# Performance work log

Hardware: AMD Instinct MI355X
Metric: run time of the kernel (lower is better)

The kernel has to match this reference:

```python
import jax, jax.numpy as jnp
import numpy as np

D_MODEL, D_STATE, D_CONV, D_INNER, DT_RANK = 256, 128, 4, 512, 16

def _pos_encoding(L, d):
    pos = jnp.arange(L, dtype=jnp.float32)[:, None]
    div = jnp.exp(jnp.arange(0, d, 2, dtype=jnp.float32) * (-np.log(10000.0) / d))
    pe = jnp.zeros((L, d), dtype=jnp.float32)
    pe = pe.at[:, 0::2].set(jnp.sin(pos * div))
    pe = pe.at[:, 1::2].set(jnp.cos(pos * div))
    return pe

def setup_inputs() -> dict:
    key = jax.random.key(0)
    ks = jax.random.split(key, 16)
    B = 16
    s = 0.02
    inp = {
        'text': jax.random.normal(ks[0], (B, 768), jnp.float32),
        'img': jax.random.normal(ks[1], (B, 1568, 196), jnp.float32),
        'first_hidden': jax.random.normal(ks[2], (B, 3584), jnp.float32),
        'last_hidden': jax.random.normal(ks[3], (B, 3584), jnp.float32),
        'pt_w': jax.random.normal(ks[4], (D_MODEL, 768), jnp.float32) * s,
        'pt_b': jnp.zeros((D_MODEL,), jnp.float32),
        'pi_w': jax.random.normal(ks[5], (D_MODEL, 1568), jnp.float32) * s,
        'pi_b': jnp.zeros((D_MODEL,), jnp.float32),
        'pf_w': jax.random.normal(ks[6], (D_MODEL, 3584), jnp.float32) * s,
        'pf_b': jnp.zeros((D_MODEL,), jnp.float32),
        'pl_w': jax.random.normal(ks[7], (D_MODEL, 3584), jnp.float32) * s,
        'pl_b': jnp.zeros((D_MODEL,), jnp.float32),
        'in_proj_w': jax.random.normal(ks[8], (2 * D_INNER, D_MODEL), jnp.float32) * s,
        'conv_w': jax.random.normal(ks[9], (D_INNER, D_CONV), jnp.float32) * 0.1,
        'conv_b': jnp.zeros((D_INNER,), jnp.float32),
        'x_proj_w': jax.random.normal(ks[10], (DT_RANK + 2 * D_STATE, D_INNER), jnp.float32) * s,
        'dt_proj_w': jax.random.normal(ks[11], (D_INNER, DT_RANK), jnp.float32) * (DT_RANK ** -0.5),
        'dt_proj_b': jnp.log(jnp.expm1(jnp.full((D_INNER,), 0.01, jnp.float32))),
        'A_log': jnp.broadcast_to(jnp.log(jnp.arange(1, D_STATE + 1, dtype=jnp.float32)), (D_INNER, D_STATE)).copy(),
        'Dp': jnp.ones((D_INNER,), jnp.float32),
        'out_proj_w': jax.random.normal(ks[12], (D_MODEL, D_INNER), jnp.float32) * s,
    }
    return inp

def _mamba(seq, in_proj_w, conv_w, conv_b, x_proj_w, dt_proj_w, dt_proj_b, A_log, Dp, out_proj_w):
    B, L, _ = seq.shape
    xz = seq @ in_proj_w.T                       # [B, L, 2*dI]
    x, z = jnp.split(xz, 2, axis=-1)             # each [B, L, dI]
    # causal depthwise conv1d (kernel d_conv, left-pad)
    xp = jnp.pad(x, ((0, 0), (D_CONV - 1, 0), (0, 0)))
    xc = sum(xp[:, k:k + L, :] * conv_w[:, k] for k in range(D_CONV)) + conv_b
    x = jax.nn.silu(xc)
    dbc = x @ x_proj_w.T                         # [B, L, dt_rank + 2*dS]
    dt = dbc[..., :DT_RANK]
    Bm = dbc[..., DT_RANK:DT_RANK + D_STATE]
    Cm = dbc[..., DT_RANK + D_STATE:]
    delta = jax.nn.softplus(dt @ dt_proj_w.T + dt_proj_b)  # [B, L, dI]
    A = -jnp.exp(A_log)                          # [dI, dS]

    def step(h, inp):
        d_t, x_t, b_t, c_t = inp                 # [B,dI],[B,dI],[B,dS],[B,dS]
        dA = jnp.exp(d_t[..., None] * A)         # [B, dI, dS]
        h = dA * h + (d_t * x_t)[..., None] * b_t[:, None, :]
        y = jnp.einsum('bds,bs->bd', h, c_t)
        return h, y

    h0 = jnp.zeros((B, D_INNER, D_STATE), seq.dtype)
    xs = (jnp.swapaxes(delta, 0, 1), jnp.swapaxes(x, 0, 1),
          jnp.swapaxes(Bm, 0, 1), jnp.swapaxes(Cm, 0, 1))
    _, ys = jax.lax.scan(step, h0, xs)           # ys: [L, B, dI]
    y = jnp.swapaxes(ys, 0, 1) + x * Dp
    y = y * jax.nn.silu(z)
    return y @ out_proj_w.T

def reference(text, img, first_hidden, last_hidden, pt_w, pt_b, pi_w, pi_b,
              pf_w, pf_b, pl_w, pl_b, in_proj_w, conv_w, conv_b, x_proj_w,
              dt_proj_w, dt_proj_b, A_log, Dp, out_proj_w):
    t = (text @ pt_w.T + pt_b)[:, None, :]                       # [B,1,256]
    im = jnp.swapaxes(img, 1, 2) @ pi_w.T + pi_b                 # [B,196,256]
    f = (first_hidden @ pf_w.T + pf_b)[:, None, :]
    l = (last_hidden @ pl_w.T + pl_b)[:, None, :]
    seq = jnp.concatenate([t, im, f, l], axis=1)                 # [B,199,256]
    seq = seq + _pos_encoding(seq.shape[1], D_MODEL)[None]
    residual = seq
    out = _mamba(seq, in_proj_w, conv_w, conv_b, x_proj_w,
                 dt_proj_w, dt_proj_b, A_log, Dp, out_proj_w)
    return out + residual
```

## Files before the change

kernel.cpp:

```cpp
#include <hip/hip_runtime.h>
#include <hip/hip_bf16.h>
#include <math.h>

#define D_MODEL 256
#define D_STATE 128
#define D_CONV  4
#define D_INNER 512
#define DT_RANK 16
#define BATCH   16
#define LIMG    196
#define LSEQ    199
#define KTXT    768
#define KIMG    1568
#define KHID    3584
#define N_TOK   (BATCH*LSEQ)
#define N_IMG   (BATCH*LIMG)

typedef const float* fp32p;
typedef __attribute__((ext_vector_type(8))) short bf16x8;
typedef __attribute__((ext_vector_type(4))) float f32x4;
typedef __attribute__((ext_vector_type(2))) float f32x2;

__device__ __forceinline__ unsigned short f2bf(float f) {
    unsigned int u = __float_as_uint(f);
    u += 0x7FFFu + ((u >> 16) & 1u);
    return (unsigned short)(u >> 16);
}

__device__ __forceinline__ float bf2f(unsigned short u) {
    return __uint_as_float(((unsigned int)u) << 16);
}

#define KCH 256
__global__ __launch_bounds__(256) void cvt_embed_kernel(
    fp32p inp_w, fp32p pi_w, fp32p xp_w, fp32p out_w, fp32p dt_w,
    unsigned short* __restrict__ inp_o, unsigned short* __restrict__ pi_o,
    unsigned short* __restrict__ xp_o, unsigned short* __restrict__ out_o,
    unsigned short* __restrict__ dt_o,
    fp32p text, fp32p firsth, fp32p lasth,
    fp32p pt_w, fp32p pf_w, fp32p pl_w,
    float* __restrict__ ppart)
{
    __shared__ __align__(16) float As[32][20];
    __shared__ __align__(16) float Ws[32][68];
    if (blockIdx.x < 928) {
        int i = (blockIdx.x * 256 + threadIdx.x) * 4;
        if (i >= 950272) return;
        if (i >= 933888) {
            int q = (i - 933888) >> 2;
            int n = q >> 3, kq = q & 7;
            int k = 4 * kq;
            ushort4 o;
            if (k < DT_RANK) {
                float4 v = *(const float4*)(dt_w + (size_t)n * DT_RANK + k);
                o.x = f2bf(v.x); o.y = f2bf(v.y); o.z = f2bf(v.z); o.w = f2bf(v.w);
            } else { o.x = o.y = o.z = o.w = 0; }
            *(ushort4*)(dt_o + (size_t)n * 32 + k) = o;
            return;
        }
        const float* src; unsigned short* dst; int off;
        if (i < 262144)      { src = inp_w; dst = inp_o; off = i; }
        else if (i < 663552) { src = pi_w;  dst = pi_o;  off = i - 262144; }
        else if (i < 802816) { src = xp_w;  dst = xp_o;  off = i - 663552; }
        else                 { src = out_w; dst = out_o; off = i - 802816; }
        float4 v = *(const float4*)(src + off);
        ushort4 o;
        o.x = f2bf(v.x); o.y = f2bf(v.y); o.z = f2bf(v.z); o.w = f2bf(v.w);
        *(ushort4*)(dst + off) = o;
        return;
    }
    const int q = blockIdx.x - 928;
    const int chunk = q % 31;
    const int n0 = (q / 31) * 64;
    const float *src, *w; int k0, K;
    if (chunk < 3)       { src = text;   w = pt_w; k0 = chunk*KCH;      K = KTXT; }
    else if (chunk < 17) { src = firsth; w = pf_w; k0 = (chunk-3)*KCH;  K = KHID; }
    else                 { src = lasth;  w = pl_w; k0 = (chunk-17)*KCH; K = KHID; }

    const int tid = threadIdx.x;
    const int tm = (tid & 7) * 2;
    const int tn = (tid >> 3) * 2;
    float acc[2][2] = {{0.f,0.f},{0.f,0.f}};

    for (int ks = 0; ks < KCH; ks += 32) {
        __syncthreads();
        if (tid < 128) {
            int m = tid >> 3, kq = tid & 7;
            float4 v = *(const float4*)(src + (size_t)m*K + k0 + ks + 4*kq);
            As[4*kq+0][m]=v.x; As[4*kq+1][m]=v.y; As[4*kq+2][m]=v.z; As[4*kq+3][m]=v.w;
        }
        for (int f = tid; f < 512; f += 256) {
            int n = f >> 3, kq = f & 7;
            float4 v = *(const float4*)(w + (size_t)(n0+n)*K + k0 + ks + 4*kq);
            Ws[4*kq+0][n]=v.x; Ws[4*kq+1][n]=v.y; Ws[4*kq+2][n]=v.z; Ws[4*kq+3][n]=v.w;
        }
        __syncthreads();
        #pragma unroll
        for (int kk = 0; kk < 32; ++kk) {
            float2 a = *(const float2*)&As[kk][tm];
            float2 b = *(const float2*)&Ws[kk][tn];
            acc[0][0] = fmaf(a.x, b.x, acc[0][0]);
            acc[0][1] = fmaf(a.x, b.y, acc[0][1]);
            acc[1][0] = fmaf(a.y, b.x, acc[1][0]);
            acc[1][1] = fmaf(a.y, b.y, acc[1][1]);
        }
    }
    float* pp = ppart + (size_t)chunk*16*256;
    pp[(size_t)(tm+0)*256 + n0+tn+0] = acc[0][0];
    pp[(size_t)(tm+0)*256 + n0+tn+1] = acc[0][1];
    pp[(size_t)(tm+1)*256 + n0+tn+0] = acc[1][0];
    pp[(size_t)(tm+1)*256 + n0+tn+1] = acc[1][1];
}

__global__ __launch_bounds__(256) void mfma_dt_kernel(
    const float* __restrict__ dbc,
    const unsigned short* __restrict__ Wbf,
    fp32p dt_b, float* __restrict__ delta_T, float* __restrict__ rr_T)
{
    const int w    = threadIdx.x >> 6;
    const int lane = threadIdx.x & 63;
    const int m0   = blockIdx.x * 64 + 16 * w;
    const int n0   = blockIdx.y * 32;
    const int r15  = lane & 15;
    const int quad = lane >> 4;

    f32x4 acc0 = {0.f,0.f,0.f,0.f}, acc1 = {0.f,0.f,0.f,0.f};

    bf16x8 a = {0,0,0,0,0,0,0,0};
    if (quad < 2) {
        int m = m0 + r15;
        if (m >= N_TOK) m = N_TOK - 1;
        const float* ap = dbc + (size_t)m * 272 + quad * 8;
        float4 v0 = *(const float4*)(ap);
        float4 v1 = *(const float4*)(ap + 4);
        a[0] = (short)f2bf(v0.x); a[1] = (short)f2bf(v0.y);
        a[2] = (short)f2bf(v0.z); a[3] = (short)f2bf(v0.w);
        a[4] = (short)f2bf(v1.x); a[5] = (short)f2bf(v1.y);
        a[6] = (short)f2bf(v1.z); a[7] = (short)f2bf(v1.w);
    }
    bf16x8 b0 = *(const bf16x8*)(Wbf + (size_t)(n0 + r15     ) * 32 + quad * 8);
    bf16x8 b1 = *(const bf16x8*)(Wbf + (size_t)(n0 + r15 + 16) * 32 + quad * 8);
    acc0 = __builtin_amdgcn_mfma_f32_16x16x32_bf16(a, b0, acc0, 0, 0, 0);
    acc1 = __builtin_amdgcn_mfma_f32_16x16x32_bf16(a, b1, acc1, 0, 0, 0);

    const int mst = m0 + quad * 4;
    const int nst = n0 + r15;
    f32x4* accs[2] = {&acc0, &acc1};
    #pragma unroll
    for (int j = 0; j < 2; ++j) {
        int n = nst + 16 * j;
        float bias = dt_b[n];
        float4 o, ro;
        float* ov = &o.x; float* rv = &ro.x;
        #pragma unroll
        for (int r = 0; r < 4; ++r) {
            float v = (*accs[j])[r] + bias;
            float dlt = (v > 20.f) ? v : log1pf(__expf(v));
            ov[r] = dlt;
            rv[r] = __expf(-dlt);
        }
        if (mst + 3 < N_TOK) {
            *(float4*)(delta_T + (size_t)n * N_TOK + mst) = o;
            *(float4*)(rr_T    + (size_t)n * N_TOK + mst) = ro;
        } else {
            #pragma unroll
            for (int r = 0; r < 4; ++r)
                if (mst + r < N_TOK) {
                    delta_T[(size_t)n * N_TOK + mst + r] = ov[r];
                    rr_T   [(size_t)n * N_TOK + mst + r] = rv[r];
                }
        }
    }
}

__global__ __launch_bounds__(256) void mfma_inproj_kernel(
    const unsigned short* __restrict__ Abf,
    const unsigned short* __restrict__ Wbf,
    float* __restrict__ C, int ldc,
    fp32p conv_w, fp32p conv_b, float* __restrict__ xs_T)
{
    __shared__ __align__(16) unsigned short Ws[64][280];
    const int tid  = threadIdx.x;
    const int w    = tid >> 6;
    const int lane = tid & 63;
    const int mb   = blockIdx.x * 64;
    const int m0   = mb + 16 * w;
    const int n0   = blockIdx.y * 64;
    const int r15  = lane & 15;
    const int quad = lane >> 4;

    for (int f = tid; f < 64*32; f += 256) {
        int row = f >> 5, col = (f & 31) * 8;
        *(bf16x8*)&Ws[row][col] =
            *(const bf16x8*)(Wbf + (size_t)(n0 + row) * 256 + col);
    }
    __syncthreads();

    f32x4 acc0 = {0.f,0.f,0.f,0.f}, acc1 = {0.f,0.f,0.f,0.f};
    f32x4 acc2 = {0.f,0.f,0.f,0.f}, acc3 = {0.f,0.f,0.f,0.f};

    const unsigned short* Ap = Abf + (size_t)(m0 + r15) * 256 + quad * 8;

    #pragma unroll
    for (int k0 = 0; k0 < 256; k0 += 32) {
        bf16x8 a  = *(const bf16x8*)(Ap + k0);
        bf16x8 b0 = *(const bf16x8*)&Ws[r15     ][k0 + quad*8];
        bf16x8 b1 = *(const bf16x8*)&Ws[r15 + 16][k0 + quad*8];
        bf16x8 b2 = *(const bf16x8*)&Ws[r15 + 32][k0 + quad*8];
        bf16x8 b3 = *(const bf16x8*)&Ws[r15 + 48][k0 + quad*8];
        acc0 = __builtin_amdgcn_mfma_f32_16x16x32_bf16(a, b0, acc0, 0, 0, 0);
        acc1 = __builtin_amdgcn_mfma_f32_16x16x32_bf16(a, b1, acc1, 0, 0, 0);
        acc2 = __builtin_amdgcn_mfma_f32_16x16x32_bf16(a, b2, acc2, 0, 0, 0);
        acc3 = __builtin_amdgcn_mfma_f32_16x16x32_bf16(a, b3, acc3, 0, 0, 0);
    }

    if (n0 >= D_INNER) {
        if (m0 < N_TOK) {
            int mst = m0 + quad * 4;
            int nst = n0 + r15;
            *(float4*)(C + (size_t)(nst     ) * ldc + mst) = *(float4*)&acc0;
            *(float4*)(C + (size_t)(nst + 16) * ldc + mst) = *(float4*)&acc1;
            *(float4*)(C + (size_t)(nst + 32) * ldc + mst) = *(float4*)&acc2;
            *(float4*)(C + (size_t)(nst + 48) * ldc + mst) = *(float4*)&acc3;
        }
        return;
    }

    float halo = 0.f;
    const int htok = tid >> 6;
    const int hch  = tid & 63;
    const bool hthr = (tid < 192);
    const bool do_h = hthr && (blockIdx.x > 0);
    if (do_h) {
        int hm = mb - 3 + htok;
        const unsigned short* ar = Abf + (size_t)hm * 256;
        const unsigned short* wr = &Ws[hch][0];
        float s = 0.f;
        for (int k = 0; k < 256; k += 8) {
            bf16x8 av = *(const bf16x8*)(ar + k);
            bf16x8 wv = *(const bf16x8*)(wr + k);
            #pragma unroll
            for (int jj = 0; jj < 8; ++jj)
                s = fmaf(bf2f((unsigned short)av[jj]),
                         bf2f((unsigned short)wv[jj]), s);
        }
        halo = s;
    }
    __syncthreads();

    float* xcs = (float*)&Ws[0][0];
    #pragma unroll
    for (int r = 0; r < 4; ++r) {
        int ml = 16*w + quad*4 + r;
        xcs[(3 + ml)*68 + r15     ] = acc0[r];
        xcs[(3 + ml)*68 + r15 + 16] = acc1[r];
        xcs[(3 + ml)*68 + r15 + 32] = acc2[r];
        xcs[(3 + ml)*68 + r15 + 48] = acc3[r];
    }
    if (hthr) xcs[htok*68 + hch] = do_h ? halo : 0.f;
    __syncthreads();

    const int mst_l = 16*w + quad*4;
    #pragma unroll
    for (int j = 0; j < 4; ++j) {
        int n = n0 + r15 + 16*j;
        const int cc = r15 + 16*j;
        float w0 = conv_w[n*D_CONV + 0], w1 = conv_w[n*D_CONV + 1];
        float w2 = conv_w[n*D_CONV + 2], w3 = conv_w[n*D_CONV + 3];
        float cb = conv_b[n];
        float4 o;
        float* ov = &o.x;
        #pragma unroll
        for (int r = 0; r < 4; ++r) {
            int ml = mst_l + r;
            int m  = mb + ml;
            int tt = m % LSEQ;
            float acc = fmaf(xcs[(3+ml  )*68 + cc], w3, cb);
            if (tt >= 1) acc = fmaf(xcs[(3+ml-1)*68 + cc], w2, acc);
            if (tt >= 2) acc = fmaf(xcs[(3+ml-2)*68 + cc], w1, acc);
            if (tt >= 3) acc = fmaf(xcs[(3+ml-3)*68 + cc], w0, acc);
            float sig = 1.f / (1.f + __expf(-acc));
            ov[r] = acc * sig;
        }
        int m = mb + mst_l;
        if (m < N_TOK) {
            if (m + 3 < N_TOK) {
                *(float4*)(xs_T + (size_t)n * N_TOK + m) = o;
            } else {
                #pragma unroll
                for (int r = 0; r < 4; ++r)
                    if (m + r < N_TOK) xs_T[(size_t)n * N_TOK + m + r] = ov[r];
            }
        }
    }
}

__global__ __launch_bounds__(256) void mfma_kt_kernel(
    const float* __restrict__ Akt, int lda,
    const unsigned short* __restrict__ Wbf, int K,
    float* __restrict__ C, int ldc, int M, int N)
{
    __shared__ __align__(16) unsigned short As[2][64][40];
    const int m0 = blockIdx.x * 64;
    const int n0 = blockIdx.y * 32;
    const int tid = threadIdx.x;
    const int w = tid >> 6, lane = tid & 63;
    const int r15 = lane & 15, quad = lane >> 4;

    const int kk0 = tid >> 4,          mq0 = tid & 15;
    const int kk1 = (tid + 256) >> 4,  mq1 = (tid + 256) & 15;
    const int sm0 = m0 + 4 * mq0, sm1 = m0 + 4 * mq1;

    f32x4 acc0 = {0.f,0.f,0.f,0.f}, acc1 = {0.f,0.f,0.f,0.f};

    const unsigned short* Wp = Wbf + (size_t)(n0 + r15) * K + quad * 8;

    {
        float4 v0 = make_float4(0.f,0.f,0.f,0.f), v1 = v0;
        if (sm0 < M) v0 = *(const float4*)(Akt + (size_t)kk0 * lda + sm0);
        if (sm1 < M) v1 = *(const float4*)(Akt + (size_t)kk1 * lda + sm1);
        As[0][4*mq0+0][kk0] = f2bf(v0.x); As[0][4*mq0+1][kk0] = f2bf(v0.y);
        As[0][4*mq0+2][kk0] = f2bf(v0.z); As[0][4*mq0+3][kk0] = f2bf(v0.w);
        As[0][4*mq1+0][kk1] = f2bf(v1.x); As[0][4*mq1+1][kk1] = f2bf(v1.y);
        As[0][4*mq1+2][kk1] = f2bf(v1.z); As[0][4*mq1+3][kk1] = f2bf(v1.w);
    }
    __syncthreads();

    int p = 0;
    for (int k0 = 0; k0 < K; k0 += 32) {
        const bool hn = (k0 + 32 < K);
        float4 nv0 = make_float4(0.f,0.f,0.f,0.f), nv1 = nv0;
        if (hn) {
            if (sm0 < M) nv0 = *(const float4*)(Akt + (size_t)(k0 + 32 + kk0) * lda + sm0);
            if (sm1 < M) nv1 = *(const float4*)(Akt + (size_t)(k0 + 32 + kk1) * lda + sm1);
        }
        bf16x8 a  = *(const bf16x8*)&As[p][16*w + r15][quad * 8];
        bf16x8 b0 = *(const bf16x8*)(Wp + k0);
        bf16x8 b1 = *(const bf16x8*)(Wp + (size_t)16*K + k0);
        acc0 = __builtin_amdgcn_mfma_f32_16x16x32_bf16(a, b0, acc0, 0, 0, 0);
        acc1 = __builtin_amdgcn_mfma_f32_16x16x32_bf16(a, b1, acc1, 0, 0, 0);
        if (hn) {
            int q = p ^ 1;
            As[q][4*mq0+0][kk0] = f2bf(nv0.x); As[q][4*mq0+1][kk0] = f2bf(nv0.y);
            As[q][4*mq0+2][kk0] = f2bf(nv0.z); As[q][4*mq0+3][kk0] = f2bf(nv0.w);
            As[q][4*mq1+0][kk1] = f2bf(nv1.x); As[q][4*mq1+1][kk1] = f2bf(nv1.y);
            As[q][4*mq1+2][kk1] = f2bf(nv1.z); As[q][4*mq1+3][kk1] = f2bf(nv1.w);
        }
        __syncthreads();
        p ^= 1;
    }

    const int nb = n0 + r15;
    #pragma unroll
    for (int r = 0; r < 4; ++r) {
        int m = m0 + 16*w + quad*4 + r;
        if (m >= M) continue;
        float* cm = C + (size_t)m * ldc;
        if (nb      < N) cm[nb     ] = acc0[r];
        if (nb + 16 < N) cm[nb + 16] = acc1[r];
    }
}

__global__ __launch_bounds__(256) void mfma_out_kernel(
    const float* __restrict__ Akt,
    const unsigned short* __restrict__ Wbf,
    const float* __restrict__ seq,
    float* __restrict__ out)
{
    __shared__ __align__(16) unsigned short As[2][64][40];
    const int m0 = blockIdx.x * 64;
    const int n0 = blockIdx.y * 32;
    const int tid = threadIdx.x;
    const int w = tid >> 6, lane = tid & 63;
    const int r15 = lane & 15, quad = lane >> 4;

    const int kk0 = tid >> 4,          mq0 = tid & 15;
    const int kk1 = (tid + 256) >> 4,  mq1 = (tid + 256) & 15;
    const int sm0 = m0 + 4 * mq0, sm1 = m0 + 4 * mq1;

    f32x4 acc0 = {0.f,0.f,0.f,0.f}, acc1 = {0.f,0.f,0.f,0.f};

    const unsigned short* Wp = Wbf + (size_t)(n0 + r15) * D_INNER + quad * 8;

    {
        float4 v0 = make_float4(0.f,0.f,0.f,0.f), v1 = v0;
        if (sm0 < N_TOK) v0 = *(const float4*)(Akt + (size_t)kk0 * N_TOK + sm0);
        if (sm1 < N_TOK) v1 = *(const float4*)(Akt + (size_t)kk1 * N_TOK + sm1);
        As[0][4*mq0+0][kk0] = f2bf(v0.x); As[0][4*mq0+1][kk0] = f2bf(v0.y);
        As[0][4*mq0+2][kk0] = f2bf(v0.z); As[0][4*mq0+3][kk0] = f2bf(v0.w);
        As[0][4*mq1+0][kk1] = f2bf(v1.x); As[0][4*mq1+1][kk1] = f2bf(v1.y);
        As[0][4*mq1+2][kk1] = f2bf(v1.z); As[0][4*mq1+3][kk1] = f2bf(v1.w);
    }
    __syncthreads();

    int p = 0;
    for (int k0 = 0; k0 < D_INNER; k0 += 32) {
        const bool hn = (k0 + 32 < D_INNER);
        float4 nv0 = make_float4(0.f,0.f,0.f,0.f), nv1 = nv0;
        if (hn) {
            if (sm0 < N_TOK) nv0 = *(const float4*)(Akt + (size_t)(k0 + 32 + kk0) * N_TOK + sm0);
            if (sm1 < N_TOK) nv1 = *(const float4*)(Akt + (size_t)(k0 + 32 + kk1) * N_TOK + sm1);
        }
        bf16x8 a  = *(const bf16x8*)&As[p][16*w + r15][quad * 8];
        bf16x8 b0 = *(const bf16x8*)(Wp + k0);
        bf16x8 b1 = *(const bf16x8*)(Wp + (size_t)16*D_INNER + k0);
        acc0 = __builtin_amdgcn_mfma_f32_16x16x32_bf16(a, b0, acc0, 0, 0, 0);
        acc1 = __builtin_amdgcn_mfma_f32_16x16x32_bf16(a, b1, acc1, 0, 0, 0);
        if (hn) {
            int q = p ^ 1;
            As[q][4*mq0+0][kk0] = f2bf(nv0.x); As[q][4*mq0+1][kk0] = f2bf(nv0.y);
            As[q][4*mq0+2][kk0] = f2bf(nv0.z); As[q][4*mq0+3][kk0] = f2bf(nv0.w);
            As[q][4*mq1+0][kk1] = f2bf(nv1.x); As[q][4*mq1+1][kk1] = f2bf(nv1.y);
            As[q][4*mq1+2][kk1] = f2bf(nv1.z); As[q][4*mq1+3][kk1] = f2bf(nv1.w);
        }
        __syncthreads();
        p ^= 1;
    }

    const int nb = n0 + r15;
    #pragma unroll
    for (int r = 0; r < 4; ++r) {
        int m = m0 + 16*w + quad*4 + r;
        if (m >= N_TOK) continue;
        const float* sm = seq + (size_t)m * D_MODEL;
        float* om = out + (size_t)m * D_MODEL;
        om[nb     ] = acc0[r] + sm[nb     ];
        om[nb + 16] = acc1[r] + sm[nb + 16];
    }
}

__global__ __launch_bounds__(256) void mfma_img_kernel(
    fp32p img, const unsigned short* __restrict__ Wbf, float* __restrict__ epart)
{
    __shared__ __align__(16) unsigned short As[2][64][40];
    __shared__ __align__(16) unsigned short Ws[64][232];
    const int b  = blockIdx.x >> 2;
    const int p0 = (blockIdx.x & 3) * 64;
    const int n0 = blockIdx.y * 64;
    const int z  = blockIdx.z;
    const int tid = threadIdx.x;
    const int w = tid >> 6, lane = tid & 63;
    const int r15 = lane & 15, quad = lane >> 4;

    const int kbeg = (z == 0) ? 0 : 416 + 384 * (z - 1);
    const int kend = kbeg + ((z == 0) ? 416 : 384);
    const int hs1    = ((kend - kbeg) >> 5) >> 1;
    const int hsplit = kbeg + hs1 * 32;

    const int kk0 = tid >> 4,          pq0 = tid & 15;
    const int kk1 = (tid + 256) >> 4,  pq1 = (tid + 256) & 15;
    const int sp0 = p0 + 4 * pq0, sp1 = p0 + 4 * pq1;

    f32x4 acc0 = {0.f,0.f,0.f,0.f}, acc1 = {0.f,0.f,0.f,0.f};
    f32x4 acc2 = {0.f,0.f,0.f,0.f}, acc3 = {0.f,0.f,0.f,0.f};

    const float* imgb = img + (size_t)b * KIMG * LIMG;

    {
        float4 v0 = make_float4(0.f,0.f,0.f,0.f), v1 = v0;
        if (sp0 < LIMG) v0 = *(const float4*)(imgb + (size_t)(kbeg + kk0) * LIMG + sp0);
        if (sp1 < LIMG) v1 = *(const float4*)(imgb + (size_t)(kbeg + kk1) * LIMG + sp1);
        As[0][4*pq0+0][kk0] = f2bf(v0.x); As[0][4*pq0+1][kk0] = f2bf(v0.y);
        As[0][4*pq0+2][kk0] = f2bf(v0.z); As[0][4*pq0+3][kk0] = f2bf(v0.w);
        As[0][4*pq1+0][kk1] = f2bf(v1.x); As[0][4*pq1+1][kk1] = f2bf(v1.y);
        As[0][4*pq1+2][kk1] = f2bf(v1.z); As[0][4*pq1+3][kk1] = f2bf(v1.w);

        int cols8 = hs1 * 4;
        int tot = 64 * cols8;
        for (int f = tid; f < tot; f += 256) {
            int row = f / cols8, col = (f % cols8) * 8;
            *(bf16x8*)&Ws[row][col] =
                *(const bf16x8*)(Wbf + (size_t)(n0 + row) * KIMG + kbeg + col);
        }
    }
    __syncthreads();

    int p = 0;
    int wsbase = kbeg;
    for (int k0 = kbeg; k0 < kend; k0 += 32) {
        const bool hn = (k0 + 32 < kend);
        float4 nv0 = make_float4(0.f,0.f,0.f,0.f), nv1 = nv0;
        if (hn) {
            if (sp0 < LIMG) nv0 = *(const float4*)(imgb + (size_t)(k0 + 32 + kk0) * LIMG + sp0);
            if (sp1 < LIMG) nv1 = *(const float4*)(imgb + (size_t)(k0 + 32 + kk1) * LIMG + sp1);
        }
        const int wc = (k0 - wsbase) + quad * 8;
        bf16x8 a  = *(const bf16x8*)&As[p][16*w + r15][quad * 8];
        bf16x8 b0 = *(const bf16x8*)&Ws[r15     ][wc];
        bf16x8 b1 = *(const bf16x8*)&Ws[r15 + 16][wc];
        bf16x8 b2 = *(const bf16x8*)&Ws[r15 + 32][wc];
        bf16x8 b3 = *(const bf16x8*)&Ws[r15 + 48][wc];
        acc0 = __builtin_amdgcn_mfma_f32_16x16x32_bf16(a, b0, acc0, 0, 0, 0);
        acc1 = __builtin_amdgcn_mfma_f32_16x16x32_bf16(a, b1, acc1, 0, 0, 0);
        acc2 = __builtin_amdgcn_mfma_f32_16x16x32_bf16(a, b2, acc2, 0, 0, 0);
        acc3 = __builtin_amdgcn_mfma_f32_16x16x32_bf16(a, b3, acc3, 0, 0, 0);
        if (hn) {
            int q = p ^ 1;
            As[q][4*pq0+0][kk0] = f2bf(nv0.x); As[q][4*pq0+1][kk0] = f2bf(nv0.y);
            As[q][4*pq0+2][kk0] = f2bf(nv0.z); As[q][4*pq0+3][kk0] = f2bf(nv0.w);
            As[q][4*pq1+0][kk1] = f2bf(nv1.x); As[q][4*pq1+1][kk1] = f2bf(nv1.y);
            As[q][4*pq1+2][kk1] = f2bf(nv1.z); As[q][4*pq1+3][kk1] = f2bf(nv1.w);
        }
        __syncthreads();
        if (k0 + 32 == hsplit) {
            int cols8 = ((kend - hsplit) >> 5) * 4;
            int tot = 64 * cols8;
            for (int f = tid; f < tot; f += 256) {
                int row = f / cols8, col = (f % cols8) * 8;
                *(bf16x8*)&Ws[row][col] =
                    *(const bf16x8*)(Wbf + (size_t)(n0 + row) * KIMG + hsplit + col);
            }
            __syncthreads();
            wsbase = hsplit;
        }
        p ^= 1;
    }

    float* ep = epart + (size_t)z * N_IMG * D_MODEL;
    #pragma unroll
    for (int r = 0; r < 4; ++r) {
        int pp = p0 + 16*w + quad*4 + r;
        if (pp >= LIMG) continue;
        size_t base = ((size_t)b * LIMG + pp) * D_MODEL + n0 + r15;
        ep[base     ] = acc0[r];
        ep[base + 16] = acc1[r];
        ep[base + 32] = acc2[r];
        ep[base + 48] = acc3[r];
    }
}

__global__ __launch_bounds__(256) void finish_all_kernel(
    const float* __restrict__ epart, fp32p pi_b,
    const float* __restrict__ ppart, fp32p pt_b, fp32p pf_b, fp32p pl_b,
    float* __restrict__ seq, unsigned short* __restrict__ seq_bf)
{
    const float cpe = -9.210340371976184f / 256.0f;
    if (blockIdx.x < 784) {
        int idx = (blockIdx.x * 256 + threadIdx.x) * 4;
        int d0  = idx & (D_MODEL - 1);
        int row = idx >> 8;
        int b = row / LIMG, p = row % LIMG;
        int l = p + 1;

        float4 a0 = *(const float4*)(epart + idx);
        float4 a1 = *(const float4*)(epart + (size_t)N_IMG * D_MODEL + idx);
        float4 a2 = *(const float4*)(epart + (size_t)2 * N_IMG * D_MODEL + idx);
        float4 a3 = *(const float4*)(epart + (size_t)3 * N_IMG * D_MODEL + idx);
        float4 bb = *(const float4*)(pi_b + d0);

        float diva = __expf((float)d0 * cpe);
        float divb = __expf((float)(d0 + 2) * cpe);
        float4 o;
        o.x = (a0.x + a1.x) + (a2.x + a3.x) + bb.x + sinf((float)l * diva);
        o.y = (a0.y + a1.y) + (a2.y + a3.y) + bb.y + cosf((float)l * diva);
        o.z = (a0.z + a1.z) + (a2.z + a3.z) + bb.z + sinf((float)l * divb);
        o.w = (a0.w + a1.w) + (a2.w + a3.w) + bb.w + cosf((float)l * divb);
        size_t off = ((size_t)b * LSEQ + l) * D_MODEL + d0;
        *(float4*)(seq + off) = o;
        ushort4 ob; ob.x = f2bf(o.x); ob.y = f2bf(o.y); ob.z = f2bf(o.z); ob.w = f2bf(o.w);
        *(ushort4*)(seq_bf + off) = ob;
    } else {
        int j = (blockIdx.x - 784) * 256 + threadIdx.x;
        if (j >= 48 * 64) return;
        int d0 = (j & 63) * 4;
        int bc = j >> 6;
        int b = bc / 3, c = bc % 3;
        int c0, nch, l; const float* bias;
        if (c == 0)      { c0 = 0;  nch = 3;  l = 0;        bias = pt_b; }
        else if (c == 1) { c0 = 3;  nch = 14; l = LIMG+1;   bias = pf_b; }
        else             { c0 = 17; nch = 14; l = LIMG+2;   bias = pl_b; }
        float4 s = *(const float4*)(bias + d0);
        for (int ch = 0; ch < nch; ++ch) {
            float4 v = *(const float4*)(ppart + (size_t)(c0+ch)*16*256 + (size_t)b*256 + d0);
            s.x += v.x; s.y += v.y; s.z += v.z; s.w += v.w;
        }
        float diva = __expf((float)d0 * cpe);
        float divb = __expf((float)(d0 + 2) * cpe);
        s.x += sinf((float)l * diva);
        s.y += cosf((float)l * diva);
        s.z += sinf((float)l * divb);
        s.w += cosf((float)l * divb);
        size_t off = ((size_t)b * LSEQ + l) * D_MODEL + d0;
        *(float4*)(seq + off) = s;
        ushort4 ob; ob.x = f2bf(s.x); ob.y = f2bf(s.y); ob.z = f2bf(s.z); ob.w = f2bf(s.w);
        *(ushort4*)(seq_bf + off) = ob;
    }
}

#define TCH   16
#define NFULL 48

__global__ __launch_bounds__(256) void scan_kernel(
    const float* __restrict__ delta_T, const float* __restrict__ xs_T,
    const float* __restrict__ xz_T, const float* __restrict__ dbc_ws,
    const float* __restrict__ rr_T,
    fp32p A_log, fp32p Dp, float* __restrict__ y_T)
{
    __shared__ __align__(16) float part[4][TCH][68];
    __shared__ __align__(16) float stage[2][4][256];
    __shared__ __align__(16) float dlx[2][96];

    const int wv   = threadIdx.x >> 6;
    const int lane = threadIdx.x & 63;
    const int tid  = threadIdx.x;
    const int wid  = blockIdx.x*4 + wv;
    const int b  = wid >> 8;
    const int dp = wid & 255;
    const int sl = lane & 31;
    const int ch = lane >> 5;
    const int d  = dp*2 + ch;
    const int ch8 = (wv << 1) | ch;
    const int base_d = ((blockIdx.x*4) & 255) * 2;

    const float L2E  = 1.4426950408889634f;
    const float A0L  = -__expf(A_log[(size_t)d*D_STATE + 4*sl]) * L2E;
    const float nL2E = -L2E;

    const float* dl   = delta_T + (size_t)d*N_TOK + b*LSEQ;
    const float* xl   = xs_T    + (size_t)d*N_TOK + b*LSEQ;
    const float* dbc0 = dbc_ws  + (size_t)b*LSEQ*272 + DT_RANK;
    float* pw = &part[wv][0][0];

    const float Dr = Dp[d];
    const float* zr = xz_T + (size_t)(D_INNER + d)*N_TOK + b*LSEQ;
    float*       yr = y_T  + (size_t)d*N_TOK + b*LSEQ;

    const int  sidx = tid - 64;
    const bool do_s = (tid >= 64 && tid < 160);
    const int  s_arr = sidx >> 5, s_c8 = (sidx >> 2) & 7, s_j = sidx & 3;
    const float* s_arrp = (s_arr == 0) ? delta_T : (s_arr == 1 ? xs_T : rr_T);
    const float* s_base = s_arrp + (size_t)(base_d + s_c8)*N_TOK + b*LSEQ + s_j;

    f32x2 h01 = {0.f, 0.f}, h23 = {0.f, 0.f};

    {
        float4 bc0 = *(const float4*)(dbc0 + (size_t)wv*272 + 4*lane);
        *(float4*)&stage[0][wv][4*lane] = bc0;
        if (do_s) dlx[0][sidx] = s_base[0];
    }
    __syncthreads();

    float xt = 0.f, zt = 0.f;
    int cur = 0;
    for (int g = 0; g < NFULL; ++g) {
        const int gg = g & 3;
        if (gg == 0 && sl < TCH) {
            int t = (g >> 2)*TCH + sl;
            xt = xl[t]; zt = zr[t];
        }
        float4 bcN = *(const float4*)(dbc0 + (size_t)(4*(g+1) + wv)*272 + 4*lane);
        float dlxN = 0.f;
        if (do_s) dlxN = s_base[4*(g+1)];

        float4 dv4 = *(const float4*)&dlx[cur][     ch8*4];
        float4 xv4 = *(const float4*)&dlx[cur][32 + ch8*4];
        float4 rv4 = *(const float4*)&dlx[cur][64 + ch8*4];
        const float* sb = &stage[cur][0][0];
        #pragma unroll
        for (int j = 0; j < 4; ++j) {
            float D  = ((const float*)&dv4)[j];
            float X  = ((const float*)&xv4)[j];
            float rr = ((const float*)&rv4)[j];
            float4 Bq = *(const float4*)(sb + j*256 + 4*sl);
            float4 Cq = *(const float4*)(sb + j*256 + 128 + 4*sl);
            float du = D * X;
            float e0;
            asm("v_exp_f32 %0, %1" : "=v"(e0) : "v"(D * A0L));
            float rr2 = rr * rr;
            f32x2 e01 = {e0, e0 * rr};
            f32x2 e23 = e01 * rr2;
            f32x2 B01 = {Bq.x, Bq.y}, B23 = {Bq.z, Bq.w};
            f32x2 C01 = {Cq.x, Cq.y}, C23 = {Cq.z, Cq.w};
            h01 = e01 * h01 + du * B01;
            h23 = e23 * h23 + du * B23;
            f32x2 p2 = h01 * C01 + h23 * C23;
            pw[(gg*4 + j)*68 + lane] = p2.x + p2.y;
        }
        if (gg == 3 && sl < TCH) {
            const float* pr = pw + sl*68 + ch*32;
            float s0 = 0.f, s1 = 0.f;
            #pragma unroll
            for (int k = 0; k < 32; k += 8) {
                float4 v0 = *(const float4*)(pr + k);
                float4 v1 = *(const float4*)(pr + k + 4);
                s0 += (v0.x + v0.y) + (v0.z + v0.w);
                s1 += (v1.x + v1.y) + (v1.z + v1.w);
            }
            int t = (g >> 2)*TCH + sl;
            float y = fmaf(xt, Dr, s0 + s1);
            yr[t] = y * (zt / (1.f + __expf(-zt)));
        }
        *(float4*)&stage[cur^1][wv][4*lane] = bcN;
        if (do_s) dlx[cur^1][sidx] = dlxN;
        __syncthreads();
        cur ^= 1;
    }

    {
        const int t0 = NFULL*4, tc = LSEQ - t0;
        float xt2 = 0.f, zt2 = 0.f;
        if (sl < tc) { xt2 = xl[t0 + sl]; zt2 = zr[t0 + sl]; }
        for (int tt = 0; tt < tc; ++tt) {
            const int t = t0 + tt;
            float D = dl[t], X = xl[t];
            const float* r = dbc0 + (size_t)t*272 + 4*sl;
            float4 Bq = *(const float4*)(r);
            float4 Cq = *(const float4*)(r + D_STATE);
            float du = D * X;
            float e0, rr;
            asm("v_exp_f32 %0, %1" : "=v"(e0) : "v"(D * A0L));
            asm("v_exp_f32 %0, %1" : "=v"(rr) : "v"(D * nL2E));
            float rr2 = rr * rr;
            f32x2 e01 = {e0, e0 * rr};
            f32x2 e23 = e01 * rr2;
            f32x2 B01 = {Bq.x, Bq.y}, B23 = {Bq.z, Bq.w};
            f32x2 C01 = {Cq.x, Cq.y}, C23 = {Cq.z, Cq.w};
            h01 = e01 * h01 + du * B01;
            h23 = e23 * h23 + du * B23;
            f32x2 p2 = h01 * C01 + h23 * C23;
            pw[tt*68 + lane] = p2.x + p2.y;
        }
        if (sl < tc) {
            const float* pr = pw + sl*68 + ch*32;
            float s0 = 0.f, s1 = 0.f;
            #pragma unroll
            for (int k = 0; k < 32; k += 8) {
                float4 v0 = *(const float4*)(pr + k);
                float4 v1 = *(const float4*)(pr + k + 4);
                s0 += (v0.x + v0.y) + (v0.z + v0.w);
                s1 += (v1.x + v1.y) + (v1.z + v1.w);
            }
            float y = fmaf(xt2, Dr, s0 + s1);
            yr[t0 + sl] = y * (zt2 / (1.f + __expf(-zt2)));
        }
    }
}

extern "C" void kernel_launch(void* const* d_in, const int* in_sizes, int n_in,
                              void* d_out, int out_size, void* d_ws, size_t ws_size,
                              hipStream_t stream)
{
    fp32p text   = (fp32p)d_in[0];
    fp32p img    = (fp32p)d_in[1];
    fp32p firsth = (fp32p)d_in[2];
    fp32p lasth  = (fp32p)d_in[3];
    fp32p pt_w   = (fp32p)d_in[4];
    fp32p pt_b   = (fp32p)d_in[5];
    fp32p pi_w   = (fp32p)d_in[6];
    fp32p pi_b   = (fp32p)d_in[7];
    fp32p pf_w   = (fp32p)d_in[8];
    fp32p pf_b   = (fp32p)d_in[9];
    fp32p pl_w   = (fp32p)d_in[10];
    fp32p pl_b   = (fp32p)d_in[11];
    fp32p inp_w  = (fp32p)d_in[12];
    fp32p conv_w = (fp32p)d_in[13];
    fp32p conv_b = (fp32p)d_in[14];
    fp32p xp_w   = (fp32p)d_in[15];
    fp32p dt_w   = (fp32p)d_in[16];
    fp32p dt_b   = (fp32p)d_in[17];
    fp32p A_log  = (fp32p)d_in[18];
    fp32p Dp     = (fp32p)d_in[19];
    fp32p out_w  = (fp32p)d_in[20];

    float* ws      = (float*)d_ws;
    float* seq     = ws;
    float* xz_T    = seq     + (size_t)N_TOK*D_MODEL;
    float* xs_T    = xz_T    + (size_t)1024*N_TOK + 16;
    float* dbc_ws  = xs_T    + (size_t)D_INNER*N_TOK + 16;
    float* delta_T = dbc_ws  + (size_t)N_TOK*272;
    float* y_T     = delta_T + (size_t)D_INNER*N_TOK + 16;
    float* epart   = y_T     + (size_t)D_INNER*N_TOK + 16;
    float* ppart   = epart   + (size_t)4*N_IMG*D_MODEL;
    unsigned short* seq_bf   = (unsigned short*)(ppart + (size_t)31*16*256);
    unsigned short* inp_wbf  = seq_bf  + (size_t)3200*D_MODEL;
    unsigned short* pi_wbf   = inp_wbf + (size_t)1024*D_MODEL;
    unsigned short* xp_wbf   = pi_wbf  + (size_t)D_MODEL*KIMG;
    unsigned short* out_wbf  = xp_wbf  + (size_t)320*D_INNER;
    unsigned short* dt_wbf   = out_wbf + (size_t)D_MODEL*D_INNER;

    float* rr_T = epart;

    cvt_embed_kernel<<<1052, 256, 0, stream>>>(
        inp_w, pi_w, xp_w, out_w, dt_w, inp_wbf, pi_wbf, xp_wbf, out_wbf, dt_wbf,
        text, firsth, lasth, pt_w, pf_w, pl_w, ppart);

    mfma_img_kernel<<<dim3(BATCH*4, 4, 4), 256, 0, stream>>>(img, pi_wbf, epart);
    finish_all_kernel<<<796, 256, 0, stream>>>(
        epart, pi_b, ppart, pt_b, pf_b, pl_b, seq, seq_bf);

    mfma_inproj_kernel<<<dim3(50, 16), 256, 0, stream>>>(
        seq_bf, inp_wbf, xz_T, N_TOK, conv_w, conv_b, xs_T);

    mfma_kt_kernel<<<dim3(50, 9), 256, 0, stream>>>(
        xs_T, N_TOK, xp_wbf, D_INNER, dbc_ws, 272, N_TOK, 272);

    mfma_dt_kernel<<<dim3(50, 16), 256, 0, stream>>>(
        dbc_ws, dt_wbf, dt_b, delta_T, rr_T);

    scan_kernel<<<BATCH*D_INNER/8, 256, 0, stream>>>(
        delta_T, xs_T, xz_T, dbc_ws, rr_T, A_log, Dp, y_T);

    mfma_out_kernel<<<dim3(50, 8), 256, 0, stream>>>(
        y_T, out_wbf, seq, (float*)d_out);
}
```

Before: 255.5 us.

## Fold dt_proj into x_proj weights and compute delta inside x_proj GEMM

Precomputes a combined weight dt_proj_w @ x_proj_w[:16] (bf16, 512x512) in the conversion kernel. The x_proj GEMM grid is extended with extra column blocks that multiply xs directly by this combined weight and apply softplus and exp, so the separate dt kernel launch and its dependency on dbc are gone. The trade is that the delta GEMM's K grows from 16 to 512, which adds MFMA work. The combined weight is rounded to bf16 after the product, which changes numerics slightly.

After: 258.9 us. About the same (+1.3%).

```diff
diff --git a/kernel.cpp b/kernel.cpp
--- a/kernel.cpp
+++ b/kernel.cpp
@@ -36,7 +36,7 @@
     fp32p inp_w, fp32p pi_w, fp32p xp_w, fp32p out_w, fp32p dt_w,
     unsigned short* __restrict__ inp_o, unsigned short* __restrict__ pi_o,
     unsigned short* __restrict__ xp_o, unsigned short* __restrict__ out_o,
-    unsigned short* __restrict__ dt_o,
+    unsigned short* __restrict__ wcomb_o,
     fp32p text, fp32p firsth, fp32p lasth,
     fp32p pt_w, fp32p pf_w, fp32p pl_w,
     float* __restrict__ ppart)
@@ -45,19 +45,7 @@
     __shared__ __align__(16) float Ws[32][68];
     if (blockIdx.x < 928) {
         int i = (blockIdx.x * 256 + threadIdx.x) * 4;
-        if (i >= 950272) return;
-        if (i >= 933888) {
-            int q = (i - 933888) >> 2;
-            int n = q >> 3, kq = q & 7;
-            int k = 4 * kq;
-            ushort4 o;
-            if (k < DT_RANK) {
-                float4 v = *(const float4*)(dt_w + (size_t)n * DT_RANK + k);
-                o.x = f2bf(v.x); o.y = f2bf(v.y); o.z = f2bf(v.z); o.w = f2bf(v.w);
-            } else { o.x = o.y = o.z = o.w = 0; }
-            *(ushort4*)(dt_o + (size_t)n * 32 + k) = o;
-            return;
-        }
+        if (i >= 933888) return;
         const float* src; unsigned short* dst; int off;
         if (i < 262144)      { src = inp_w; dst = inp_o; off = i; }
         else if (i < 663552) { src = pi_w;  dst = pi_o;  off = i - 262144; }
@@ -69,6 +57,25 @@
         *(ushort4*)(dst + off) = o;
         return;
     }
+    if (blockIdx.x >= 1052) {
+        int o = ((blockIdx.x - 1052) * 256 + threadIdx.x) * 4;
+        int dd = o >> 9, k = o & 511;
+        float4 s = make_float4(0.f, 0.f, 0.f, 0.f);
+        const float* dw = dt_w + (size_t)dd * DT_RANK;
+        #pragma unroll
+        for (int r = 0; r < DT_RANK; ++r) {
+            float wv = dw[r];
+            const float* xr = xp_w + (size_t)r * D_INNER + k;
+            s.x = fmaf(wv, xr[0], s.x);
+            s.y = fmaf(wv, xr[1], s.y);
+            s.z = fmaf(wv, xr[2], s.z);
+            s.w = fmaf(wv, xr[3], s.w);
+        }
+        ushort4 ob;
+        ob.x = f2bf(s.x); ob.y = f2bf(s.y); ob.z = f2bf(s.z); ob.w = f2bf(s.w);
+        *(ushort4*)(wcomb_o + (size_t)dd * D_INNER + k) = ob;
+        return;
+    }
     const int q = blockIdx.x - 928;
     const int chunk = q % 31;
     const int n0 = (q / 31) * 64;
@@ -110,67 +117,6 @@
     pp[(size_t)(tm+0)*256 + n0+tn+1] = acc[0][1];
     pp[(size_t)(tm+1)*256 + n0+tn+0] = acc[1][0];
     pp[(size_t)(tm+1)*256 + n0+tn+1] = acc[1][1];
-}
-
-__global__ __launch_bounds__(256) void mfma_dt_kernel(
-    const float* __restrict__ dbc,
-    const unsigned short* __restrict__ Wbf,
-    fp32p dt_b, float* __restrict__ delta_T, float* __restrict__ rr_T)
-{
-    const int w    = threadIdx.x >> 6;
-    const int lane = threadIdx.x & 63;
-    const int m0   = blockIdx.x * 64 + 16 * w;
-    const int n0   = blockIdx.y * 32;
-    const int r15  = lane & 15;
-    const int quad = lane >> 4;
-
-    f32x4 acc0 = {0.f,0.f,0.f,0.f}, acc1 = {0.f,0.f,0.f,0.f};
-
-    bf16x8 a = {0,0,0,0,0,0,0,0};
-    if (quad < 2) {
-        int m = m0 + r15;
-        if (m >= N_TOK) m = N_TOK - 1;
-        const float* ap = dbc + (size_t)m * 272 + quad * 8;
-        float4 v0 = *(const float4*)(ap);
-        float4 v1 = *(const float4*)(ap + 4);
-        a[0] = (short)f2bf(v0.x); a[1] = (short)f2bf(v0.y);
-        a[2] = (short)f2bf(v0.z); a[3] = (short)f2bf(v0.w);
-        a[4] = (short)f2bf(v1.x); a[5] = (short)f2bf(v1.y);
-        a[6] = (short)f2bf(v1.z); a[7] = (short)f2bf(v1.w);
-    }
-    bf16x8 b0 = *(const bf16x8*)(Wbf + (size_t)(n0 + r15     ) * 32 + quad * 8);
-    bf16x8 b1 = *(const bf16x8*)(Wbf + (size_t)(n0 + r15 + 16) * 32 + quad * 8);
-    acc0 = __builtin_amdgcn_mfma_f32_16x16x32_bf16(a, b0, acc0, 0, 0, 0);
-    acc1 = __builtin_amdgcn_mfma_f32_16x16x32_bf16(a, b1, acc1, 0, 0, 0);
-
-    const int mst = m0 + quad * 4;
-    const int nst = n0 + r15;
-    f32x4* accs[2] = {&acc0, &acc1};
-    #pragma unroll
-    for (int j = 0; j < 2; ++j) {
-        int n = nst + 16 * j;
-        float bias = dt_b[n];
-        float4 o, ro;
-        float* ov = &o.x; float* rv = &ro.x;
-        #pragma unroll
-        for (int r = 0; r < 4; ++r) {
-            float v = (*accs[j])[r] + bias;
-            float dlt = (v > 20.f) ? v : log1pf(__expf(v));
-            ov[r] = dlt;
-            rv[r] = __expf(-dlt);
-        }
-        if (mst + 3 < N_TOK) {
-            *(float4*)(delta_T + (size_t)n * N_TOK + mst) = o;
-            *(float4*)(rr_T    + (size_t)n * N_TOK + mst) = ro;
-        } else {
-            #pragma unroll
-            for (int r = 0; r < 4; ++r)
-                if (mst + r < N_TOK) {
-                    delta_T[(size_t)n * N_TOK + mst + r] = ov[r];
-                    rr_T   [(size_t)n * N_TOK + mst + r] = rv[r];
-                }
-        }
-    }
 }
 
 __global__ __launch_bounds__(256) void mfma_inproj_kernel(
@@ -298,11 +244,14 @@
 __global__ __launch_bounds__(256) void mfma_kt_kernel(
     const float* __restrict__ Akt, int lda,
     const unsigned short* __restrict__ Wbf, int K,
-    float* __restrict__ C, int ldc, int M, int N)
+    float* __restrict__ C, int ldc, int M, int N,
+    const unsigned short* __restrict__ wcomb, fp32p dt_b,
+    float* __restrict__ delta_T, float* __restrict__ rr_T)
 {
     __shared__ __align__(16) unsigned short As[2][64][40];
     const int m0 = blockIdx.x * 64;
     const int n0 = blockIdx.y * 32;
+    const bool isdt = (blockIdx.y >= 9);
     const int tid = threadIdx.x;
     const int w = tid >> 6, lane = tid & 63;
     const int r15 = lane & 15, quad = lane >> 4;
@@ -313,7 +262,9 @@
 
     f32x4 acc0 = {0.f,0.f,0.f,0.f}, acc1 = {0.f,0.f,0.f,0.f};
 
-    const unsigned short* Wp = Wbf + (size_t)(n0 + r15) * K + quad * 8;
+    const unsigned short* Wp = isdt
+        ? wcomb + (size_t)(n0 - 288 + r15) * D_INNER + quad * 8
+        : Wbf   + (size_t)(n0 + r15) * K + quad * 8;
 
     {
         float4 v0 = make_float4(0.f,0.f,0.f,0.f), v1 = v0;
@@ -336,7 +287,7 @@
         }
         bf16x8 a  = *(const bf16x8*)&As[p][16*w + r15][quad * 8];
         bf16x8 b0 = *(const bf16x8*)(Wp + k0);
-        bf16x8 b1 = *(const bf16x8*)(Wp + (size_t)16*K + k0);
+        bf16x8 b1 = *(const bf16x8*)(Wp + (size_t)16*D_INNER + k0);
         acc0 = __builtin_amdgcn_mfma_f32_16x16x32_bf16(a, b0, acc0, 0, 0, 0);
         acc1 = __builtin_amdgcn_mfma_f32_16x16x32_bf16(a, b1, acc1, 0, 0, 0);
         if (hn) {
@@ -350,14 +301,45 @@
         p ^= 1;
     }
 
-    const int nb = n0 + r15;
-    #pragma unroll
-    for (int r = 0; r < 4; ++r) {
-        int m = m0 + 16*w + quad*4 + r;
-        if (m >= M) continue;
-        float* cm = C + (size_t)m * ldc;
-        if (nb      < N) cm[nb     ] = acc0[r];
-        if (nb + 16 < N) cm[nb + 16] = acc1[r];
+    if (!isdt) {
+        const int nb = n0 + r15;
+        #pragma unroll
+        for (int r = 0; r < 4; ++r) {
+            int m = m0 + 16*w + quad*4 + r;
+            if (m >= M) continue;
+            float* cm = C + (size_t)m * ldc;
+            if (nb      < N) cm[nb     ] = acc0[r];
+            if (nb + 16 < N) cm[nb + 16] = acc1[r];
+        }
+    } else {
+        const int mst = m0 + 16*w + quad*4;
+        const int nst = (n0 - 288) + r15;
+        f32x4* accs[2] = {&acc0, &acc1};
+        #pragma unroll
+        for (int j = 0; j < 2; ++j) {
+            int n = nst + 16 * j;
+            float bias = dt_b[n];
+            float4 o, ro;
+            float* ov = &o.x; float* rv = &ro.x;
+            #pragma unroll
+            for (int r = 0; r < 4; ++r) {
+                float v = (*accs[j])[r] + bias;
+                float dlt = (v > 20.f) ? v : log1pf(__expf(v));
+                ov[r] = dlt;
+                rv[r] = __expf(-dlt);
+            }
+            if (mst + 3 < N_TOK) {
+                *(float4*)(delta_T + (size_t)n * N_TOK + mst) = o;
+                *(float4*)(rr_T    + (size_t)n * N_TOK + mst) = ro;
+            } else {
+                #pragma unroll
+                for (int r = 0; r < 4; ++r)
+                    if (mst + r < N_TOK) {
+                        delta_T[(size_t)n * N_TOK + mst + r] = ov[r];
+                        rr_T   [(size_t)n * N_TOK + mst + r] = rv[r];
+                    }
+            }
+        }
     }
 }
 
@@ -776,13 +758,13 @@
     unsigned short* pi_wbf   = inp_wbf + (size_t)1024*D_MODEL;
     unsigned short* xp_wbf   = pi_wbf  + (size_t)D_MODEL*KIMG;
     unsigned short* out_wbf  = xp_wbf  + (size_t)320*D_INNER;
-    unsigned short* dt_wbf   = out_wbf + (size_t)D_MODEL*D_INNER;
+    unsigned short* wcomb_bf = out_wbf + (size_t)D_MODEL*D_INNER;
 
     float* rr_T = epart;
 
-    cvt_embed_kernel<<<1052, 256, 0, stream>>>(
-        inp_w, pi_w, xp_w, out_w, dt_w, inp_wbf, pi_wbf, xp_wbf, out_wbf, dt_wbf,
-        text, firsth, lasth, pt_w, pf_w, pl_w, ppart);
+    cvt_embed_kernel<<<1308, 256, 0, stream>>>(
+        inp_w, pi_w, xp_w, out_w, dt_w, inp_wbf, pi_wbf, xp_wbf, out_wbf,
+        wcomb_bf, text, firsth, lasth, pt_w, pf_w, pl_w, ppart);
 
     mfma_img_kernel<<<dim3(BATCH*4, 4, 4), 256, 0, stream>>>(img, pi_wbf, epart);
     finish_all_kernel<<<796, 256, 0, stream>>>(
@@ -791,11 +773,9 @@
     mfma_inproj_kernel<<<dim3(50, 16), 256, 0, stream>>>(
         seq_bf, inp_wbf, xz_T, N_TOK, conv_w, conv_b, xs_T);
 
-    mfma_kt_kernel<<<dim3(50, 9), 256, 0, stream>>>(
-        xs_T, N_TOK, xp_wbf, D_INNER, dbc_ws, 272, N_TOK, 272);
-
-    mfma_dt_kernel<<<dim3(50, 16), 256, 0, stream>>>(
-        dbc_ws, dt_wbf, dt_b, delta_T, rr_T);
+    mfma_kt_kernel<<<dim3(50, 25), 256, 0, stream>>>(
+        xs_T, N_TOK, xp_wbf, D_INNER, dbc_ws, 272, N_TOK, 272,
+        wcomb_bf, dt_b, delta_T, rr_T);
 
     scan_kernel<<<BATCH*D_INNER/8, 256, 0, stream>>>(
         delta_T, xs_T, xz_T, dbc_ws, rr_T, A_log, Dp, y_T);
```
